# Optimization experiments

Measured on AMD Instinct MI355X. Metric: run time of the kernel, lower is better.

The kernel has to match this reference:

```python
import jax, jax.numpy as jnp
import numpy as np

N_NODES = 100000
N_EDGES = 1000000
IN_CH = 64
HID = 128
OUT_CH = 2
N_GRAPHS = 256


def setup_inputs() -> dict:
    key = jax.random.key(0)
    ks = jax.random.split(key, 12)
    x = jax.random.normal(ks[0], (N_NODES, IN_CH), dtype=jnp.float32)
    edge_index = jax.random.randint(ks[1], (2, N_EDGES), 0, N_NODES, dtype=jnp.int64)
    batch = jnp.sort(jax.random.randint(ks[2], (N_NODES,), 0, N_GRAPHS, dtype=jnp.int64))
    def glorot(k, shape):
        lim = float(np.sqrt(6.0 / (shape[0] + shape[1])))
        return jax.random.uniform(k, shape, dtype=jnp.float32, minval=-lim, maxval=lim)
    # SAGEConv: out = lin_l(mean_agg(x_j)) + lin_r(x_i); bias on lin_l only (PyG default)
    Wl1 = glorot(ks[3], (HID, IN_CH))
    bl1 = jnp.zeros((HID,), dtype=jnp.float32)
    Wr1 = glorot(ks[4], (HID, IN_CH))
    Wl2 = glorot(ks[5], (HID, HID))
    bl2 = jnp.zeros((HID,), dtype=jnp.float32)
    Wr2 = glorot(ks[6], (HID, HID))
    Wout = glorot(ks[7], (OUT_CH, HID))
    bout = jnp.zeros((OUT_CH,), dtype=jnp.float32)
    return {"x": x, "edge_index": edge_index, "batch": batch,
            "Wl1": Wl1, "bl1": bl1, "Wr1": Wr1,
            "Wl2": Wl2, "bl2": bl2, "Wr2": Wr2,
            "Wout": Wout, "bout": bout}


def _sage_conv(x, src, dst, Wl, bl, Wr):
    # mean-aggregate source features onto target nodes, then two linears
    msgs = x[src]                                                # [E, d]
    agg = jax.ops.segment_sum(msgs, dst, num_segments=N_NODES)  # [N, d]
    deg = jax.ops.segment_sum(jnp.ones((src.shape[0], 1), x.dtype), dst,
                              num_segments=N_NODES)             # [N, 1]
    agg = agg / jnp.maximum(deg, 1.0)
    return agg @ Wl.T + bl + x @ Wr.T


def reference(x, edge_index, batch, Wl1, bl1, Wr1, Wl2, bl2, Wr2, Wout, bout):
    src, dst = edge_index[0], edge_index[1]
    h = jax.nn.relu(_sage_conv(x, src, dst, Wl1, bl1, Wr1))
    # dropout(p=0.2) is identity in eval mode
    h = jax.nn.relu(_sage_conv(h, src, dst, Wl2, bl2, Wr2))
    # global_mean_pool over graph ids
    pooled = jax.ops.segment_sum(h, batch, num_segments=N_GRAPHS)      # [G, H]
    cnt = jax.ops.segment_sum(jnp.ones((h.shape[0], 1), h.dtype), batch,
                              num_segments=N_GRAPHS)                   # [G, 1]
    pooled = pooled / jnp.maximum(cnt, 1.0)
    logits = pooled @ Wout.T + bout
    return jax.nn.log_softmax(logits, axis=1)
```

## Files before the change

### kernel.cpp

```cpp
#include <hip/hip_runtime.h>
#include <hip/hip_bf16.h>
#include <math.h>

typedef short short8_t __attribute__((ext_vector_type(8)));
typedef float floatx4  __attribute__((ext_vector_type(4)));
typedef float floatx2  __attribute__((ext_vector_type(2)));
typedef unsigned int uint;

#define EPB 1024
#define BSH 9


__device__ inline unsigned short f2b(float f) {
    uint u = __float_as_uint(f);
    u += 0x7fff + ((u >> 16) & 1);
    return (unsigned short)(u >> 16);
}
__device__ inline uint pack2(float a, float b) {
    return (uint)f2b(a) | ((uint)f2b(b) << 16);
}


__device__ inline uint enc4_fp8(float f0, float f1, float f2, float f3) {
    uint v = __builtin_amdgcn_cvt_pk_fp8_f32(f0, f1, 0, false);
    v = __builtin_amdgcn_cvt_pk_fp8_f32(f2, f3, v, true);
    return v;
}
__device__ inline unsigned char enc1_fp8(float f) {
    return (unsigned char)(__builtin_amdgcn_cvt_pk_fp8_f32(f, f, 0, false) & 0xff);
}



__device__ inline void scan256(int* ss, int t) {
#pragma unroll
    for (int off = 1; off < 256; off <<= 1) {
        int u = (t >= off) ? ss[t - off] : 0;
        __syncthreads();
        ss[t] += u;
        __syncthreads();
    }
}

__global__ __launch_bounds__(256) void k_phase_a(
    const int* __restrict__ dst, int* __restrict__ bhist, int E,
    const float* __restrict__ x, unsigned short* __restrict__ xb,
    unsigned char* __restrict__ xf8, int nX,
    const float* __restrict__ Wl1, const float* __restrict__ Wr1,
    const float* __restrict__ Wl2, const float* __restrict__ Wr2,
    unsigned short* __restrict__ wbuf,
    float* __restrict__ pooled,
    const int* __restrict__ batch, int* __restrict__ gstart, int N, int G,
    int bHist, int bCvtX, int bCvtW, int bZero) {
    __shared__ int h[256];
    int b = blockIdx.x;
    int tid = threadIdx.x;
    if (b < bHist) {
        h[tid] = 0;
        __syncthreads();
        int e = b * EPB + tid * 4;
        if (e + 3 < E) {
            int4 d4 = *(const int4*)(dst + e);
            atomicAdd(&h[d4.x >> BSH], 1);
            atomicAdd(&h[d4.y >> BSH], 1);
            atomicAdd(&h[d4.z >> BSH], 1);
            atomicAdd(&h[d4.w >> BSH], 1);
        } else {
            for (int k = e; k < E; ++k) atomicAdd(&h[dst[k] >> BSH], 1);
        }
        __syncthreads();
        bhist[(size_t)b * 256 + tid] = h[tid];
    } else if (b < bHist + bCvtX) {
        int i = ((b - bHist) * 256 + tid) * 8;
        if (i < nX) {
            float4 v0 = *(const float4*)(x + i);
            float4 v1 = *(const float4*)(x + i + 4);
            uint4 ob;
            ob.x = pack2(v0.x, v0.y);
            ob.y = pack2(v0.z, v0.w);
            ob.z = pack2(v1.x, v1.y);
            ob.w = pack2(v1.z, v1.w);
            *(uint4*)(xb + i) = ob;
            uint2 of;
            of.x = enc4_fp8(v0.x, v0.y, v0.z, v0.w);
            of.y = enc4_fp8(v1.x, v1.y, v1.z, v1.w);
            *(uint2*)(xf8 + i) = of;
        }
    } else if (b < bHist + bCvtX + bCvtW) {
        int i = (b - bHist - bCvtX) * 256 + tid;
        if (i < 49152) {
            float v;
            if (i < 8192)       v = Wl1[i];
            else if (i < 16384) v = Wr1[i - 8192];
            else if (i < 32768) v = Wl2[i - 16384];
            else                v = Wr2[i - 32768];
            wbuf[i] = f2b(v);
        }
    } else if (b < bHist + bCvtX + bCvtW + bZero) {
        int i = ((b - bHist - bCvtX - bCvtW) * 256 + tid) * 4;
        float4 z = make_float4(0.f, 0.f, 0.f, 0.f);
        *(float4*)(pooled + i) = z;
    } else {
        for (int g = tid; g <= G; g += 256) {
            if (g == G) { gstart[G] = N; continue; }
            int lo = 0, hi = N;
            while (lo < hi) {
                int mid = (lo + hi) >> 1;
                if (batch[mid] < g) lo = mid + 1; else hi = mid;
            }
            gstart[g] = lo;
        }
    }
}

__global__ __launch_bounds__(256) void k_scan_bh(int* __restrict__ bhist,
                                                 int* __restrict__ btot, int nb) {
    __shared__ int ss[256];
    int k = blockIdx.x;
    int t = threadIdx.x;
    int b0 = t * 4;
    int v[4];
    int sum = 0;
#pragma unroll
    for (int i = 0; i < 4; ++i) {
        int b = b0 + i;
        v[i] = (b < nb) ? bhist[(size_t)b * 256 + k] : 0;
        sum += v[i];
    }
    ss[t] = sum;
    __syncthreads();
    scan256(ss, t);
    int run = ss[t] - sum;
#pragma unroll
    for (int i = 0; i < 4; ++i) {
        int b = b0 + i;
        if (b < nb) { bhist[(size_t)b * 256 + k] = run; run += v[i]; }
    }
    if (t == 0) btot[k] = ss[255];
}

__global__ __launch_bounds__(256) void k_scatter_b(
    const int* __restrict__ src, const int* __restrict__ dst,
    const int* __restrict__ bhist, const int* __restrict__ btot,
    int* __restrict__ ebuf, int E) {
    __shared__ int ss[256];
    __shared__ int lbase[256];
    int b = blockIdx.x;
    int t = threadIdx.x;
    int v = btot[t];
    ss[t] = v;
    __syncthreads();
    scan256(ss, t);
    lbase[t] = (ss[t] - v) + bhist[(size_t)b * 256 + t];
    __syncthreads();
    int e = b * EPB + t * 4;
    if (e + 3 < E) {
        int4 d4 = *(const int4*)(dst + e);
        int4 s4 = *(const int4*)(src + e);
        int k, p;
        k = d4.x >> BSH; p = atomicAdd(&lbase[k], 1); ebuf[p] = ((d4.x & 511) << 23) | s4.x;
        k = d4.y >> BSH; p = atomicAdd(&lbase[k], 1); ebuf[p] = ((d4.y & 511) << 23) | s4.y;
        k = d4.z >> BSH; p = atomicAdd(&lbase[k], 1); ebuf[p] = ((d4.z & 511) << 23) | s4.z;
        k = d4.w >> BSH; p = atomicAdd(&lbase[k], 1); ebuf[p] = ((d4.w & 511) << 23) | s4.w;
    } else {
        for (int q = e; q < E; ++q) {
            int d = dst[q];
            int p = atomicAdd(&lbase[d >> BSH], 1);
            ebuf[p] = ((d & 511) << 23) | src[q];
        }
    }
}

__global__ __launch_bounds__(256) void k_bucket_csr(
    const int* __restrict__ ebuf, const int* __restrict__ btot,
    int* __restrict__ row_start, int* __restrict__ csr_src, int N, int NB) {
    __shared__ int ss[256];
    __shared__ int bbS[257];
    __shared__ int h2[512];
    int k = blockIdx.x;
    int t = threadIdx.x;
    int v = btot[t];
    ss[t] = v;
    __syncthreads();
    scan256(ss, t);
    bbS[t] = ss[t] - v;
    if (t == 255) bbS[256] = ss[255];
    __syncthreads();
    int s = bbS[k], e = bbS[k + 1];
    int node0 = k << BSH;
    int nn = N - node0; if (nn > 512) nn = 512;
    if (k == NB - 1 && t == 0) row_start[node0 + nn] = e;
    h2[t] = 0; h2[t + 256] = 0;
    __syncthreads();
    for (int i = s + t; i < e; i += 256)
        atomicAdd(&h2[((uint)ebuf[i]) >> 23], 1);
    __syncthreads();
    int a0 = h2[2 * t], a1 = h2[2 * t + 1];
    int ps = a0 + a1;
    ss[t] = ps;
    __syncthreads();
    scan256(ss, t);
    int base = ss[t] - ps;
    h2[2 * t] = base;
    h2[2 * t + 1] = base + a0;
    __syncthreads();
    int rs0 = h2[t];
    int rs1 = h2[t + 256];
    __syncthreads();
    if (t < nn)       row_start[node0 + t]       = s + rs0;
    if (t + 256 < nn) row_start[node0 + t + 256] = s + rs1;
    for (int i = s + t; i < e; i += 256) {
        int rec = ebuf[i];
        int j = ((uint)rec) >> 23;
        int pos = atomicAdd(&h2[j], 1);
        csr_src[s + pos] = rec & 0x7FFFFF;
    }
}


#define ACCF8(v)                                                        \
    { floatx2 f = __builtin_amdgcn_cvt_pk_f32_fp8((v).x, false);        \
      a[0] += f[0]; a[1] += f[1];                                       \
      f = __builtin_amdgcn_cvt_pk_f32_fp8((v).x, true);                 \
      a[2] += f[0]; a[3] += f[1];                                       \
      f = __builtin_amdgcn_cvt_pk_f32_fp8((v).y, false);                \
      a[4] += f[0]; a[5] += f[1];                                       \
      f = __builtin_amdgcn_cvt_pk_f32_fp8((v).y, true);                 \
      a[6] += f[0]; a[7] += f[1]; }

__global__ void k_gather1(const unsigned char* __restrict__ xf8,
                          const int* __restrict__ row_start,
                          const int* __restrict__ csr_src,
                          unsigned short* __restrict__ agg, int n_nodes) {
    int tid = threadIdx.x;
    int node = blockIdx.x * 32 + (tid >> 3);
    if (node >= n_nodes) return;
    int lp = tid & 7;
    int s = row_start[node];
    int e = row_start[node + 1];
    float a[8];
#pragma unroll
    for (int q = 0; q < 8; ++q) a[q] = 0.f;
    int i = s;
    for (; i + 1 < e; i += 2) {
        int u0 = csr_src[i];
        int u1 = csr_src[i + 1];
        uint2 v0 = *(const uint2*)(xf8 + (size_t)u0 * 64 + lp * 8);
        uint2 v1 = *(const uint2*)(xf8 + (size_t)u1 * 64 + lp * 8);
        ACCF8(v0);
        ACCF8(v1);
    }
    if (i < e) {
        int u0 = csr_src[i];
        uint2 v0 = *(const uint2*)(xf8 + (size_t)u0 * 64 + lp * 8);
        ACCF8(v0);
    }
    int d = e - s;
    float scale = (d > 0) ? (1.f / (float)d) : 1.f;
    uint4 o;
    o.x = pack2(a[0] * scale, a[1] * scale);
    o.y = pack2(a[2] * scale, a[3] * scale);
    o.z = pack2(a[4] * scale, a[5] * scale);
    o.w = pack2(a[6] * scale, a[7] * scale);
    *(uint4*)(agg + (size_t)node * 64 + lp * 8) = o;
}

__global__ void k_gather2(const unsigned char* __restrict__ h1f8,
                          const int* __restrict__ row_start,
                          const int* __restrict__ csr_src,
                          unsigned short* __restrict__ agg, int n_nodes) {
    int tid = threadIdx.x;
    int node = blockIdx.x * 16 + (tid >> 4);
    if (node >= n_nodes) return;
    int lp = tid & 15;
    int s = row_start[node];
    int e = row_start[node + 1];
    float a[8];
#pragma unroll
    for (int q = 0; q < 8; ++q) a[q] = 0.f;
    int i = s;
    for (; i + 1 < e; i += 2) {
        int u0 = csr_src[i];
        int u1 = csr_src[i + 1];
        uint2 v0 = *(const uint2*)(h1f8 + (size_t)u0 * 128 + lp * 8);
        uint2 v1 = *(const uint2*)(h1f8 + (size_t)u1 * 128 + lp * 8);
        ACCF8(v0);
        ACCF8(v1);
    }
    if (i < e) {
        int u0 = csr_src[i];
        uint2 v0 = *(const uint2*)(h1f8 + (size_t)u0 * 128 + lp * 8);
        ACCF8(v0);
    }
    int d = e - s;
    float scale = (d > 0) ? (1.f / (float)d) : 1.f;
    uint4 o;
    o.x = pack2(a[0] * scale, a[1] * scale);
    o.y = pack2(a[2] * scale, a[3] * scale);
    o.z = pack2(a[4] * scale, a[5] * scale);
    o.w = pack2(a[6] * scale, a[7] * scale);
    *(uint4*)(agg + (size_t)node * 128 + lp * 8) = o;
}


template <int K, bool POOL>
__global__ __launch_bounds__(256) void k_linear_mfma(
    const unsigned short* __restrict__ aggA, const unsigned short* __restrict__ xinA,
    const unsigned short* __restrict__ Wlb,  const float* __restrict__ bl,
    const unsigned short* __restrict__ Wrb,  unsigned short* __restrict__ out,
    unsigned char* __restrict__ outf8,
    const int* __restrict__ batch, float* __restrict__ pooled, int n_nodes) {
    constexpr int NCH = (2 * K) / 32;
    constexpr int KP = K + 8;
    constexpr int SLOTS = K / 8;
    __shared__ __align__(16) short As[2 * 128 * KP];
    __shared__ int bb[128];

    int tid  = threadIdx.x;
    int lane = tid & 63;
    int wave = tid >> 6;
    int quad = lane >> 4;
    int lr   = lane & 15;
    int node0 = blockIdx.x * 128;

    if (POOL && tid < 128) {
        int n = node0 + tid;
        bb[tid] = (n < n_nodes) ? batch[n] : 0;
    }

#pragma unroll
    for (int idx = tid; idx < 128 * SLOTS; idx += 256) {
        int row  = idx / SLOTS;
        int slot = idx % SLOTS;
        int n = node0 + row; if (n >= n_nodes) n = n_nodes - 1;
        uint4 va = *(const uint4*)(aggA + (size_t)n * K + slot * 8);
        uint4 vx = *(const uint4*)(xinA + (size_t)n * K + slot * 8);
        *(uint4*)(&As[row * KP + slot * 8]) = va;
        *(uint4*)(&As[128 * KP + row * KP + slot * 8]) = vx;
    }
    __syncthreads();

    floatx4 acc[8][2];
#pragma unroll
    for (int mi = 0; mi < 8; ++mi)
#pragma unroll
        for (int ni = 0; ni < 2; ++ni)
            acc[mi][ni] = (floatx4){0.f, 0.f, 0.f, 0.f};

#pragma unroll
    for (int c = 0; c < NCH; ++c) {
        const unsigned short* srcW = (c < K / 32) ? Wlb : Wrb;
        int base = (c < K / 32) ? 0 : 128 * KP;
        int kb   = (c < K / 32) ? c * 32 : (c - K / 32) * 32;

        short8_t bfrag[2];
#pragma unroll
        for (int ni = 0; ni < 2; ++ni) {
            int j = wave * 32 + ni * 16 + lr;
            bfrag[ni] = *(const short8_t*)(srcW + (size_t)j * K + kb + quad * 8);
        }
#pragma unroll
        for (int mi = 0; mi < 8; ++mi) {
            short8_t af = *(const short8_t*)(&As[base + (mi * 16 + lr) * KP + kb + quad * 8]);
            acc[mi][0] = __builtin_amdgcn_mfma_f32_16x16x32_bf16(af, bfrag[0], acc[mi][0], 0, 0, 0);
            acc[mi][1] = __builtin_amdgcn_mfma_f32_16x16x32_bf16(af, bfrag[1], acc[mi][1], 0, 0, 0);
        }
    }

    float b0 = bl[wave * 32 + lr];
    float b1 = bl[wave * 32 + 16 + lr];
    int j0 = wave * 32 + lr;

    if (!POOL) {
#pragma unroll
        for (int mi = 0; mi < 8; ++mi) {
#pragma unroll
            for (int r = 0; r < 4; ++r) {
                int node = node0 + mi * 16 + quad * 4 + r;
                if (node < n_nodes) {
                    float v0 = fmaxf(acc[mi][0][r] + b0, 0.f);
                    float v1 = fmaxf(acc[mi][1][r] + b1, 0.f);
                    out[(size_t)node * 128 + j0]      = f2b(v0);
                    out[(size_t)node * 128 + j0 + 16] = f2b(v1);
                    outf8[(size_t)node * 128 + j0]      = enc1_fp8(v0);
                    outf8[(size_t)node * 128 + j0 + 16] = enc1_fp8(v1);
                }
            }
        }
    } else {
        int gcur = -1;
        float s0 = 0.f, s1 = 0.f;
#pragma unroll
        for (int mi = 0; mi < 8; ++mi) {
#pragma unroll
            for (int r = 0; r < 4; ++r) {
                int li = mi * 16 + quad * 4 + r;
                int node = node0 + li;
                if (node < n_nodes) {
                    float v0 = fmaxf(acc[mi][0][r] + b0, 0.f);
                    float v1 = fmaxf(acc[mi][1][r] + b1, 0.f);
                    int g = bb[li];
                    if (g != gcur) {
                        if (gcur >= 0) {
                            atomicAdd(&pooled[gcur * 128 + j0], s0);
                            atomicAdd(&pooled[gcur * 128 + j0 + 16], s1);
                        }
                        gcur = g; s0 = 0.f; s1 = 0.f;
                    }
                    s0 += v0;
                    s1 += v1;
                }
            }
        }
        if (gcur >= 0) {
            atomicAdd(&pooled[gcur * 128 + j0], s0);
            atomicAdd(&pooled[gcur * 128 + j0 + 16], s1);
        }
    }
}


__global__ void k_head(const float* __restrict__ pooled,
                       const int* __restrict__ gstart,
                       const float* __restrict__ Wout,
                       const float* __restrict__ bout,
                       float* __restrict__ out) {
    int g = blockIdx.x;
    int lane = threadIdx.x;
    float p0 = pooled[g * 128 + lane];
    float p1 = pooled[g * 128 + 64 + lane];
    float d0 = p0 * Wout[lane] + p1 * Wout[64 + lane];
    float d1 = p0 * Wout[128 + lane] + p1 * Wout[192 + lane];
#pragma unroll
    for (int m = 32; m > 0; m >>= 1) {
        d0 += __shfl_xor(d0, m);
        d1 += __shfl_xor(d1, m);
    }
    if (lane == 0) {
        float cnt = (float)(gstart[g + 1] - gstart[g]);
        float inv = (cnt > 0.f) ? (1.f / cnt) : 1.f;
        float l0 = d0 * inv + bout[0];
        float l1 = d1 * inv + bout[1];
        float mx = fmaxf(l0, l1);
        float lse = mx + logf(expf(l0 - mx) + expf(l1 - mx));
        out[g * 2 + 0] = l0 - lse;
        out[g * 2 + 1] = l1 - lse;
    }
}


static inline size_t alignUp(size_t x, size_t a) { return (x + a - 1) & ~(a - 1); }

extern "C" void kernel_launch(void* const* d_in, const int* in_sizes, int n_in,
                              void* d_out, int out_size, void* d_ws, size_t ws_size,
                              hipStream_t stream) {
    const float* x    = (const float*)d_in[0];
    const int*   ei   = (const int*)d_in[1];
    const int*   batch= (const int*)d_in[2];
    const float* Wl1  = (const float*)d_in[3];
    const float* bl1  = (const float*)d_in[4];
    const float* Wr1  = (const float*)d_in[5];
    const float* Wl2  = (const float*)d_in[6];
    const float* bl2  = (const float*)d_in[7];
    const float* Wr2  = (const float*)d_in[8];
    const float* Wout = (const float*)d_in[9];
    const float* bout = (const float*)d_in[10];
    float* out = (float*)d_out;

    const int N = in_sizes[0] / 64;
    const int E = in_sizes[1] / 2;
    const int G = out_size / 2;

    const int* src = ei;
    const int* dst = ei + E;

    const int bHist = (E + EPB - 1) / EPB;
    const int NB    = (N + 511) >> BSH;
    const int bCvtX = (N * 64 / 8 + 255) / 256;
    const int bCvtW = 192;
    const int bZero = (G * 128 / 4 + 255) / 256;

    char* ws = (char*)d_ws;
    size_t off = 0;
    int*   bhist     = (int*)(ws + off); off = alignUp(off + (size_t)bHist * 256 * 4, 256);
    int*   btot      = (int*)(ws + off); off = alignUp(off + (size_t)257 * 4, 256);
    int*   row_start = (int*)(ws + off); off = alignUp(off + (size_t)(N + 1) * 4, 256);
    int*   ebuf      = (int*)(ws + off); off = alignUp(off + (size_t)E * 4, 256);
    int*   csr_src   = (int*)(ws + off); off = alignUp(off + (size_t)E * 4, 256);
    int*   gstart    = (int*)(ws + off); off = alignUp(off + (size_t)(G + 1) * 4, 256);
    unsigned short* xb   = (unsigned short*)(ws + off); off = alignUp(off + (size_t)N * 64 * 2, 256);
    unsigned char*  xf8  = (unsigned char*)(ws + off);  off = alignUp(off + (size_t)N * 64, 256);
    unsigned short* wbuf = (unsigned short*)(ws + off); off = alignUp(off + (size_t)49152 * 2, 256);
    unsigned short* agg1 = (unsigned short*)(ws + off); off = alignUp(off + (size_t)N * 64 * 2, 256);
    unsigned short* h1   = (unsigned short*)(ws + off); off = alignUp(off + (size_t)N * 128 * 2, 256);
    unsigned char*  h1f8 = (unsigned char*)(ws + off);  off = alignUp(off + (size_t)N * 128, 256);
    unsigned short* agg2 = (unsigned short*)(ws + off); off = alignUp(off + (size_t)N * 128 * 2, 256);
    float*          pooled = (float*)(ws + off); off = alignUp(off + (size_t)G * 128 * 4, 256);
    (void)ws_size;

    unsigned short* Wl1b = wbuf;
    unsigned short* Wr1b = wbuf + 8192;
    unsigned short* Wl2b = wbuf + 16384;
    unsigned short* Wr2b = wbuf + 32768;

    k_phase_a<<<bHist + bCvtX + bCvtW + bZero + 1, 256, 0, stream>>>(
        dst, bhist, E,
        x, xb, xf8, N * 64,
        Wl1, Wr1, Wl2, Wr2, wbuf,
        pooled,
        batch, gstart, N, G,
        bHist, bCvtX, bCvtW, bZero);

    k_scan_bh<<<256, 256, 0, stream>>>(bhist, btot, bHist);
    k_scatter_b<<<bHist, 256, 0, stream>>>(src, dst, bhist, btot, ebuf, E);
    k_bucket_csr<<<NB, 256, 0, stream>>>(ebuf, btot, row_start, csr_src, N, NB);

    k_gather1<<<(N + 31) / 32, 256, 0, stream>>>(xf8, row_start, csr_src, agg1, N);
    k_linear_mfma<64, false><<<(N + 127) / 128, 256, 0, stream>>>(
        agg1, xb, Wl1b, bl1, Wr1b, h1, h1f8, nullptr, nullptr, N);

    k_gather2<<<(N + 15) / 16, 256, 0, stream>>>(h1f8, row_start, csr_src, agg2, N);
    k_linear_mfma<128, true><<<(N + 127) / 128, 256, 0, stream>>>(
        agg2, h1, Wl2b, bl2, Wr2b, nullptr, nullptr, batch, pooled, N);

    k_head<<<G, 64, 0, stream>>>(pooled, gstart, Wout, bout, out);
}
```

Measured before the change: 230.4 us.

## Unroll gathers by four and read root features straight from global in linear

The CSR gather loops now process four neighbors per iteration instead of two, which raises memory-level parallelism on random row fetches. The linear MFMA kernel no longer stages the root-node input rows in shared memory. It reads those A fragments directly from global memory in a second K loop, which halves LDS use and may raise occupancy. The cost is that each of the four waves re-reads the same x rows from global/L2 instead of sharing one LDS copy, and these loads are not coalesced.

```diff
diff --git a/kernel.cpp b/kernel.cpp
--- a/kernel.cpp
+++ b/kernel.cpp
@@ -242,15 +242,21 @@
 #pragma unroll
     for (int q = 0; q < 8; ++q) a[q] = 0.f;
     int i = s;
-    for (; i + 1 < e; i += 2) {
+    for (; i + 3 < e; i += 4) {
         int u0 = csr_src[i];
         int u1 = csr_src[i + 1];
+        int u2 = csr_src[i + 2];
+        int u3 = csr_src[i + 3];
         uint2 v0 = *(const uint2*)(xf8 + (size_t)u0 * 64 + lp * 8);
         uint2 v1 = *(const uint2*)(xf8 + (size_t)u1 * 64 + lp * 8);
+        uint2 v2 = *(const uint2*)(xf8 + (size_t)u2 * 64 + lp * 8);
+        uint2 v3 = *(const uint2*)(xf8 + (size_t)u3 * 64 + lp * 8);
         ACCF8(v0);
         ACCF8(v1);
-    }
-    if (i < e) {
+        ACCF8(v2);
+        ACCF8(v3);
+    }
+    for (; i < e; ++i) {
         int u0 = csr_src[i];
         uint2 v0 = *(const uint2*)(xf8 + (size_t)u0 * 64 + lp * 8);
         ACCF8(v0);
@@ -279,15 +285,21 @@
 #pragma unroll
     for (int q = 0; q < 8; ++q) a[q] = 0.f;
     int i = s;
-    for (; i + 1 < e; i += 2) {
+    for (; i + 3 < e; i += 4) {
         int u0 = csr_src[i];
         int u1 = csr_src[i + 1];
+        int u2 = csr_src[i + 2];
+        int u3 = csr_src[i + 3];
         uint2 v0 = *(const uint2*)(h1f8 + (size_t)u0 * 128 + lp * 8);
         uint2 v1 = *(const uint2*)(h1f8 + (size_t)u1 * 128 + lp * 8);
+        uint2 v2 = *(const uint2*)(h1f8 + (size_t)u2 * 128 + lp * 8);
+        uint2 v3 = *(const uint2*)(h1f8 + (size_t)u3 * 128 + lp * 8);
         ACCF8(v0);
         ACCF8(v1);
-    }
-    if (i < e) {
+        ACCF8(v2);
+        ACCF8(v3);
+    }
+    for (; i < e; ++i) {
         int u0 = csr_src[i];
         uint2 v0 = *(const uint2*)(h1f8 + (size_t)u0 * 128 + lp * 8);
         ACCF8(v0);
@@ -310,10 +322,10 @@
     const unsigned short* __restrict__ Wrb,  unsigned short* __restrict__ out,
     unsigned char* __restrict__ outf8,
     const int* __restrict__ batch, float* __restrict__ pooled, int n_nodes) {
-    constexpr int NCH = (2 * K) / 32;
+    constexpr int KH = K / 32;
     constexpr int KP = K + 8;
     constexpr int SLOTS = K / 8;
-    __shared__ __align__(16) short As[2 * 128 * KP];
+    __shared__ __align__(16) short As[128 * KP];
     __shared__ int bb[128];
 
     int tid  = threadIdx.x;
@@ -334,9 +346,7 @@
         int slot = idx % SLOTS;
         int n = node0 + row; if (n >= n_nodes) n = n_nodes - 1;
         uint4 va = *(const uint4*)(aggA + (size_t)n * K + slot * 8);
-        uint4 vx = *(const uint4*)(xinA + (size_t)n * K + slot * 8);
         *(uint4*)(&As[row * KP + slot * 8]) = va;
-        *(uint4*)(&As[128 * KP + row * KP + slot * 8]) = vx;
     }
     __syncthreads();
 
@@ -348,20 +358,33 @@
             acc[mi][ni] = (floatx4){0.f, 0.f, 0.f, 0.f};
 
 #pragma unroll
-    for (int c = 0; c < NCH; ++c) {
-        const unsigned short* srcW = (c < K / 32) ? Wlb : Wrb;
-        int base = (c < K / 32) ? 0 : 128 * KP;
-        int kb   = (c < K / 32) ? c * 32 : (c - K / 32) * 32;
-
+    for (int c = 0; c < KH; ++c) {
         short8_t bfrag[2];
 #pragma unroll
         for (int ni = 0; ni < 2; ++ni) {
             int j = wave * 32 + ni * 16 + lr;
-            bfrag[ni] = *(const short8_t*)(srcW + (size_t)j * K + kb + quad * 8);
+            bfrag[ni] = *(const short8_t*)(Wlb + (size_t)j * K + c * 32 + quad * 8);
         }
 #pragma unroll
         for (int mi = 0; mi < 8; ++mi) {
-            short8_t af = *(const short8_t*)(&As[base + (mi * 16 + lr) * KP + kb + quad * 8]);
+            short8_t af = *(const short8_t*)(&As[(mi * 16 + lr) * KP + c * 32 + quad * 8]);
+            acc[mi][0] = __builtin_amdgcn_mfma_f32_16x16x32_bf16(af, bfrag[0], acc[mi][0], 0, 0, 0);
+            acc[mi][1] = __builtin_amdgcn_mfma_f32_16x16x32_bf16(af, bfrag[1], acc[mi][1], 0, 0, 0);
+        }
+    }
+
+#pragma unroll
+    for (int c = 0; c < KH; ++c) {
+        short8_t bfrag[2];
+#pragma unroll
+        for (int ni = 0; ni < 2; ++ni) {
+            int j = wave * 32 + ni * 16 + lr;
+            bfrag[ni] = *(const short8_t*)(Wrb + (size_t)j * K + c * 32 + quad * 8);
+        }
+#pragma unroll
+        for (int mi = 0; mi < 8; ++mi) {
+            int n = node0 + mi * 16 + lr; if (n >= n_nodes) n = n_nodes - 1;
+            short8_t af = *(const short8_t*)(xinA + (size_t)n * K + c * 32 + quad * 8);
             acc[mi][0] = __builtin_amdgcn_mfma_f32_16x16x32_bf16(af, bfrag[0], acc[mi][0], 0, 0, 0);
             acc[mi][1] = __builtin_amdgcn_mfma_f32_16x16x32_bf16(af, bfrag[1], acc[mi][1], 0, 0, 0);
         }
```

New measurement: 248.7 us. +7.9%, slower.
